# Kernel optimization log

Hardware: AMD Instinct MI355X
Metric: run time of the kernel (lower is better)

## Reference

```python
import jax, jax.numpy as jnp
import numpy as np

VOCAB = 10000
HID = 256

def setup_inputs() -> dict:
    key = jax.random.key(0)
    ks = jax.random.split(key, 7)
    B, T = 64, 64
    input_data = jax.random.randint(ks[0], (B, T), 0, VOCAB, dtype=jnp.int32)
    targets = jax.random.randint(ks[1], (B, T), 0, VOCAB, dtype=jnp.int32)
    # Xavier-ish scaled params
    E = jax.random.normal(ks[2], (VOCAB, HID), dtype=jnp.float32) * (1.0 / np.sqrt(HID))
    W_lstm = jax.random.normal(ks[3], (2 * HID, 4 * HID), dtype=jnp.float32) * (1.0 / np.sqrt(2 * HID))
    b_lstm = jnp.zeros((4 * HID,), dtype=jnp.float32)
    W_dense = jax.random.normal(ks[4], (HID, VOCAB), dtype=jnp.float32) * (1.0 / np.sqrt(HID))
    b_dense = jnp.zeros((VOCAB,), dtype=jnp.float32)
    return {"input_data": input_data, "targets": targets, "E": E,
            "W_lstm": W_lstm, "b_lstm": b_lstm, "W_dense": W_dense, "b_dense": b_dense}

def lstm_scan(xs, W, b, h0, c0):
    # xs: [T, B, H] time-major. TF LSTMCell: gates = [x,h]@W + b, order i,j,f,o, forget_bias=1.0
    def step(carry, x):
        h, c = carry
        gates = jnp.concatenate([x, h], axis=-1) @ W + b  # [B, 4H]
        i, j, f, o = jnp.split(gates, 4, axis=-1)
        c_new = jax.nn.sigmoid(f + 1.0) * c + jax.nn.sigmoid(i) * jnp.tanh(j)
        h_new = jax.nn.sigmoid(o) * jnp.tanh(c_new)
        return (h_new, c_new), h_new
    (hT, cT), hs = jax.lax.scan(step, (h0, c0), xs)
    return hs, (hT, cT)

def reference(input_data, targets, E, W_lstm, b_lstm, W_dense, b_dense):
    B, T = input_data.shape
    inputs = E[input_data]                       # [B, T, H] embedding lookup (no dropout: eval)
    xs = jnp.transpose(inputs, (1, 0, 2))        # [T, B, H]
    h0 = jnp.zeros((B, HID), dtype=E.dtype)
    c0 = jnp.zeros((B, HID), dtype=E.dtype)
    hs, _ = lstm_scan(xs, W_lstm, b_lstm, h0, c0)  # [T, B, H]
    outputs = jnp.transpose(hs, (1, 0, 2))       # [B, T, H]
    logits = outputs @ W_dense + b_dense         # [B, T, V]
    logp = jax.nn.log_softmax(logits, axis=-1)
    ce = -jnp.take_along_axis(logp, targets[..., None].astype(jnp.int32), axis=-1)[..., 0]  # [B, T]
    perplexity = jnp.exp(ce)                     # elementwise, as in add_loss_op
    return perplexity
```

## Files before the change

### kernel.cpp

```cpp
#include <hip/hip_runtime.h>
#include <math.h>

#define VOCABN 10000
#define HIDN   256
#define GATES  1024
#define BN     64
#define TN     64
#define BT     4096
#define NCT    625

typedef unsigned int       u32;
typedef unsigned short     u16;
typedef unsigned long long u64;
typedef float v4f __attribute__((ext_vector_type(4)));
typedef short v8s __attribute__((ext_vector_type(8)));

__device__ __forceinline__ float bf2f(u16 u) {
    return __uint_as_float(((u32)u) << 16);
}
__device__ __forceinline__ u16 f2bf(float f) {
    u32 u = __float_as_uint(f);
    u += 0x7FFFu + ((u >> 16) & 1u);
    return (u16)(u >> 16);
}
__device__ __forceinline__ float fast_sigmoid(float x) {
    return 1.0f / (1.0f + __expf(-x));
}
__device__ __forceinline__ float fast_tanh(float x) {
    float e = __expf(-2.0f * fabsf(x));
    float t = (1.0f - e) / (1.0f + e);
    return copysignf(t, x);
}
__device__ __forceinline__ u64 llc_load(const u64* p) {
    return __hip_atomic_load(p, __ATOMIC_RELAXED, __HIP_MEMORY_SCOPE_AGENT);
}
__device__ __forceinline__ void llc_store(u64* p, u64 v) {
    __hip_atomic_store(p, v, __ATOMIC_RELAXED, __HIP_MEMORY_SCOPE_AGENT);
}
__device__ __forceinline__ u32 cnt_add(u32* p) {
    return __hip_atomic_fetch_add(p, 1u, __ATOMIC_RELAXED,
                                  __HIP_MEMORY_SCOPE_AGENT);
}
__device__ __forceinline__ u32 cnt_read(u32* p) {
    return __hip_atomic_load(p, __ATOMIC_RELAXED, __HIP_MEMORY_SCOPE_AGENT);
}

__device__ __forceinline__ void wfrag_dev(
    const float* __restrict__ src, u16* __restrict__ dst, int ncols, int c,
    int t, u16 lt[HIDN][16])
{
    const float* s = src + (size_t)t * ncols + c * 16;
    #pragma unroll
    for (int j4 = 0; j4 < 4; ++j4) {
        float4 v = *(const float4*)(s + j4 * 4);
        lt[t][j4*4+0] = f2bf(v.x);
        lt[t][j4*4+1] = f2bf(v.y);
        lt[t][j4*4+2] = f2bf(v.z);
        lt[t][j4*4+3] = f2bf(v.w);
    }
    __syncthreads();
    #pragma unroll
    for (int h = 0; h < 2; ++h) {
        int f = t + h * 256;
        int q = f >> 6, l = f & 63;
        int m = l & 15, kb = q * 32 + ((l >> 4) & 3) * 8;
        u32 w[4];
        #pragma unroll
        for (int j = 0; j < 4; ++j)
            w[j] = (u32)lt[kb + 2*j][m] | ((u32)lt[kb + 2*j + 1][m] << 16);
        *(uint4*)(dst + (((size_t)c * 8 + q) * 64 + l) * 8) =
            make_uint4(w[0], w[1], w[2], w[3]);
    }
}

__global__ __launch_bounds__(256) void k_wfrag2(
    const float* __restrict__ W_lstm,
    u16* __restrict__ Wxf, u16* __restrict__ Whf,
    u32* __restrict__ bar)
{
    __shared__ u16 lt[HIDN][16];
    const int bid = blockIdx.x;
    if (bid == 0) bar[threadIdx.x] = 0u;
    if (bid < 64)
        wfrag_dev(W_lstm, Wxf, GATES, bid, threadIdx.x, lt);
    else
        wfrag_dev(W_lstm + (size_t)HIDN * GATES, Whf, GATES, bid - 64,
                  threadIdx.x, lt);
}

__global__ __launch_bounds__(256) void k_wfrag3(
    const float* __restrict__ W_lstm,
    const float* __restrict__ W_dense,
    u16* __restrict__ Wxf, u16* __restrict__ Whf, u16* __restrict__ Wf,
    u32* __restrict__ bar)
{
    __shared__ u16 lt[HIDN][16];
    const int bid = blockIdx.x;
    if (bid == 0) bar[threadIdx.x] = 0u;
    if (bid < 64)
        wfrag_dev(W_lstm, Wxf, GATES, bid, threadIdx.x, lt);
    else if (bid < 128)
        wfrag_dev(W_lstm + (size_t)HIDN * GATES, Whf, GATES, bid - 64,
                  threadIdx.x, lt);
    else
        wfrag_dev(W_dense, Wf, VOCABN, bid - 128, threadIdx.x, lt);
}

__global__ __launch_bounds__(256) void k_wfrag(
    const float* __restrict__ src,
    u16*         __restrict__ dst,
    int ncols)
{
    __shared__ u16 lt[HIDN][16];
    wfrag_dev(src, dst, ncols, blockIdx.x, threadIdx.x, lt);
}

__global__ __launch_bounds__(256) void k_xgates(
    const int*   __restrict__ idx,
    const float* __restrict__ E,
    const u16*   __restrict__ Wxf,
    const float* __restrict__ bl,
    float*       __restrict__ gx)
{
    const int r0   = blockIdx.x * 16;
    const int tid  = threadIdx.x;
    const int w    = tid >> 6, lane = tid & 63;
    const int m    = lane & 15, quad = lane >> 4;

    v8s a[8];
    {
        const float* e = E + (size_t)idx[r0 + m] * HIDN + quad * 8;
        #pragma unroll
        for (int q = 0; q < 8; ++q) {
            float4 x0 = *(const float4*)(e + q * 32);
            float4 x1 = *(const float4*)(e + q * 32 + 4);
            uint4 t4 = make_uint4(
                (u32)f2bf(x0.x) | ((u32)f2bf(x0.y) << 16),
                (u32)f2bf(x0.z) | ((u32)f2bf(x0.w) << 16),
                (u32)f2bf(x1.x) | ((u32)f2bf(x1.y) << 16),
                (u32)f2bf(x1.z) | ((u32)f2bf(x1.w) << 16));
            a[q] = *(v8s*)&t4;
        }
    }

    for (int c = w; c < GATES / 16; c += 4) {
        v4f acc = {0.f, 0.f, 0.f, 0.f};
        #pragma unroll
        for (int q = 0; q < 8; ++q) {
            v8s b = *(const v8s*)(Wxf + (((size_t)c * 8 + q) * 64 + lane) * 8);
            acc = __builtin_amdgcn_mfma_f32_16x16x32_bf16(a[q], b, acc, 0, 0, 0);
        }
        const int col = c * 16 + m;
        const float bv = bl[col];
        #pragma unroll
        for (int r = 0; r < 4; ++r)
            gx[(size_t)(r0 + quad * 4 + r) * GATES + col] = acc[r] + bv;
    }
}

__global__ __launch_bounds__(256) void k_plstm(
    const u16*   __restrict__ Whf,
    const float* __restrict__ gx,
    u16*                      Hx,
    u16*         __restrict__ Hb,
    u32*                      bar)
{
    __shared__ uint4 Wl4[4 * 512];
    __shared__ float gl[4][16][16];

    const int tid  = threadIdx.x;
    const int rg   = blockIdx.x >> 4;
    const int ns   = blockIdx.x & 15;
    const int u0   = ns * 16;
    const int w    = tid >> 6;
    const int lane = tid & 63;
    const int m    = lane & 15, kq = lane >> 4;

    {
        const uint4* src = (const uint4*)Whf;
        #pragma unroll
        for (int i = 0; i < 8; ++i) {
            int e  = tid + i * 256;
            int ct = e >> 9, off = e & 511;
            Wl4[e] = src[(size_t)(ct * 16 + ns) * 512 + off];
        }
    }
    {
        float* g0 = (float*)gl;
        #pragma unroll
        for (int j = 0; j < 4; ++j) g0[tid * 4 + j] = 0.0f;
    }
    __syncthreads();

    const u16* Wl = (const u16*)Wl4;

    const int r = tid >> 4, u = tid & 15;
    const int b = rg * 16 + r;
    const float* gxp = gx + (size_t)b * TN * GATES + u0 + u;
    u16* hbp = Hb + (size_t)b * TN * HIDN + u0 + u;
    const int hxw = b * HIDN + u0 + u;
    const int aoff = (rg * 16 + m) * HIDN + kq * 8;

    float cstate = 0.0f;
    float4 gxr;
    gxr.x = gxp[0]; gxr.y = gxp[256]; gxr.z = gxp[512]; gxr.w = gxp[768];

    for (int t = 0; t < TN; ++t) {
        float4 gxn = gxr;
        if (t + 1 < TN) {
            const float* p = gxp + (size_t)(t + 1) * GATES;
            gxn.x = p[0]; gxn.y = p[256]; gxn.z = p[512]; gxn.w = p[768];
        }

        if (t > 0) {
            const u64* hsrc = (const u64*)(Hx + (t & 1) * (BN * HIDN) + aoff);
            v4f acc = {0.f, 0.f, 0.f, 0.f};
            #pragma unroll
            for (int q = 0; q < 8; ++q) {
                union { u64 d[2]; v8s v; } av;
                av.d[0] = llc_load(hsrc + q * 8);
                av.d[1] = llc_load(hsrc + q * 8 + 1);
                v8s bf = *(const v8s*)(Wl + ((w * 8 + q) * 64 + lane) * 8);
                acc = __builtin_amdgcn_mfma_f32_16x16x32_bf16(av.v, bf, acc, 0, 0, 0);
            }
            #pragma unroll
            for (int rr = 0; rr < 4; ++rr)
                gl[w][kq * 4 + rr][m] = acc[rr];
        }
        __syncthreads();

        {
            float ai = gl[0][r][u] + gxr.x;
            float aj = gl[1][r][u] + gxr.y;
            float af = gl[2][r][u] + gxr.z;
            float ao = gl[3][r][u] + gxr.w;
            float ig = fast_sigmoid(ai);
            float fg = fast_sigmoid(af + 1.0f);
            float og = fast_sigmoid(ao);
            float jt = fast_tanh(aj);
            cstate = fg * cstate + ig * jt;
            float hn = og * fast_tanh(cstate);
            u32 hv = f2bf(hn);
            hbp[(size_t)t * HIDN] = (u16)hv;

            if (t + 1 < TN) {
                u32 p1 = __shfl_down(hv, 1);
                u32 p2 = __shfl_down(hv, 2);
                u32 p3 = __shfl_down(hv, 3);
                if ((tid & 3) == 0) {
                    u64 pk = (u64)(hv | (p1 << 16))
                           | ((u64)(p2 | (p3 << 16)) << 32);
                    u64* dst = (u64*)(Hx + (((t & 1) ^ 1) * (BN * HIDN)) + hxw);
                    llc_store(dst, pk);
                }
            }
        }

        if (t + 1 < TN) {
            __syncthreads();
            if (tid == 0) {
                cnt_add(&bar[rg * 64]);
                u32 tgt = (u32)(t + 1) * 16u;
                while (cnt_read(&bar[rg * 64]) < tgt)
                    __builtin_amdgcn_s_sleep(1);
            }
            __syncthreads();
        }
        gxr = gxn;
    }
}

__global__ __launch_bounds__(256, 1) void k_dense(
    const u16*   __restrict__ Hb,
    const u16*   __restrict__ Wf,
    const float* __restrict__ bd,
    float*       __restrict__ S)
{
    __shared__ float Sl[64];
    const int bid = blockIdx.x;
    const int hv  = bid & 7;
    const int rg  = bid >> 3;
    const int r0  = rg * 64;
    const int tid = threadIdx.x;
    const int w   = tid >> 6, lane = tid & 63;
    const int m   = lane & 15, kq = lane >> 4;

    if (tid < 64) Sl[tid] = 0.0f;

    v8s a[4][8];
    #pragma unroll
    for (int rt = 0; rt < 4; ++rt) {
        const u16* hrow = Hb + (size_t)(r0 + rt * 16 + m) * HIDN + kq * 8;
        #pragma unroll
        for (int q = 0; q < 8; ++q)
            a[rt][q] = *(const v8s*)(hrow + q * 32);
    }
    __syncthreads();

    float s[4][4] = {{0.f,0.f,0.f,0.f},{0.f,0.f,0.f,0.f},
                     {0.f,0.f,0.f,0.f},{0.f,0.f,0.f,0.f}};
    const int cbeg = (hv * NCT) >> 3;
    const int cend = ((hv + 1) * NCT) >> 3;
    for (int c = cbeg + w; c < cend; c += 4) {
        v4f acc[4] = {{0.f,0.f,0.f,0.f},{0.f,0.f,0.f,0.f},
                      {0.f,0.f,0.f,0.f},{0.f,0.f,0.f,0.f}};
        #pragma unroll
        for (int q = 0; q < 8; ++q) {
            v8s bq = *(const v8s*)(Wf + (((size_t)c * 8 + q) * 64 + lane) * 8);
            #pragma unroll
            for (int rt = 0; rt < 4; ++rt)
                acc[rt] = __builtin_amdgcn_mfma_f32_16x16x32_bf16(
                              a[rt][q], bq, acc[rt], 0, 0, 0);
        }
        const float bv = bd[c * 16 + m];
        #pragma unroll
        for (int rt = 0; rt < 4; ++rt)
            #pragma unroll
            for (int r = 0; r < 4; ++r)
                s[rt][r] += __expf(acc[rt][r] + bv);
    }

    #pragma unroll
    for (int rt = 0; rt < 4; ++rt)
        #pragma unroll
        for (int r = 0; r < 4; ++r)
            atomicAdd(&Sl[rt * 16 + kq * 4 + r], s[rt][r]);
    __syncthreads();
    if (tid < 64) S[(size_t)hv * BT + r0 + tid] = Sl[tid];
}

__global__ __launch_bounds__(256) void k_target(
    const u16*   __restrict__ Hb,
    const u16*   __restrict__ Wf,
    const float* __restrict__ bd,
    const int*   __restrict__ tgt,
    const float* __restrict__ S,
    float*       __restrict__ out)
{
    const int tid = threadIdx.x;
    const int row = blockIdx.x * 8 + (tid >> 5);
    const int t   = tid & 31;
    const int q   = t >> 2, lq = t & 3;
    const int v   = tgt[row];
    const int c   = v >> 4, vm = v & 15;
    const int kb  = q * 32 + lq * 8;

    v8s h  = *(const v8s*)(Hb + (size_t)row * HIDN + kb);
    v8s wv = *(const v8s*)(Wf + (((size_t)c * 8 + q) * 64 + lq * 16 + vm) * 8);
    float acc = 0.0f;
    #pragma unroll
    for (int j = 0; j < 8; ++j)
        acc = fmaf(bf2f((u16)h[j]), bf2f((u16)wv[j]), acc);
    #pragma unroll
    for (int off = 16; off >= 1; off >>= 1)
        acc += __shfl_down(acc, off, 32);
    if (t == 0) {
        float tlv = acc + bd[v];
        float sum = 0.0f;
        #pragma unroll
        for (int p = 0; p < 8; ++p) sum += S[(size_t)p * BT + row];
        out[row] = __expf(__logf(sum) - tlv);
    }
}

extern "C" void kernel_launch(void* const* d_in, const int* in_sizes, int n_in,
                              void* d_out, int out_size, void* d_ws, size_t ws_size,
                              hipStream_t stream) {
    const int*   input   = (const int*)  d_in[0];
    const int*   targets = (const int*)  d_in[1];
    const float* E       = (const float*)d_in[2];
    const float* W_lstm  = (const float*)d_in[3];
    const float* b_lstm  = (const float*)d_in[4];
    const float* W_dense = (const float*)d_in[5];
    const float* b_dense = (const float*)d_in[6];
    float* out = (float*)d_out;

    char* ws = (char*)d_ws;
    const bool wide = (ws_size >= ((size_t)25 << 20));

    if (wide) {
        float* gx  = (float*)ws;
        u16*   Wf  = (u16*)(ws + ((size_t)16 << 20));
        u16*   Hb  = (u16*)(ws + ((size_t)21 << 20) + ((size_t)256 << 10));
        u16*   Whf = (u16*)(ws + ((size_t)23 << 20) + ((size_t)256 << 10));
        u16*   Wxf = (u16*)(ws + ((size_t)23 << 20) + ((size_t)768 << 10));
        u16*   Hx  = (u16*)(ws + ((size_t)24 << 20) + ((size_t)256 << 10));
        float* S   = (float*)(ws + ((size_t)24 << 20) + ((size_t)320 << 10));
        u32*   bar = (u32*)  (ws + ((size_t)24 << 20) + ((size_t)448 << 10));

        k_wfrag3<<<753,     256, 0, stream>>>(W_lstm, W_dense, Wxf, Whf, Wf, bar);
        k_xgates<<<BT / 16, 256, 0, stream>>>(input, E, Wxf, b_lstm, gx);
        k_plstm <<<64,      256, 0, stream>>>(Whf, gx, Hx, Hb, bar);
        k_dense <<<512,     256, 0, stream>>>(Hb, Wf, b_dense, S);
        k_target<<<BT / 8,  256, 0, stream>>>(Hb, Wf, b_dense, targets, S, out);
    } else {
        float* gx  = (float*)ws;
        u16*   Wf  = (u16*)ws;
        u16*   Hb  = (u16*)(ws + ((size_t)16 << 20));
        u16*   Whf = (u16*)(ws + ((size_t)18 << 20));
        u16*   Wxf = (u16*)(ws + ((size_t)18 << 20) + ((size_t)512 << 10));
        u16*   Hx  = (u16*)(ws + ((size_t)19 << 20));
        float* S   = (float*)(ws + ((size_t)19 << 20) + ((size_t)64 << 10));
        u32*   bar = (u32*)  (ws + ((size_t)19 << 20) + ((size_t)192 << 10));

        k_wfrag2<<<128,     256, 0, stream>>>(W_lstm, Wxf, Whf, bar);
        k_xgates<<<BT / 16, 256, 0, stream>>>(input, E, Wxf, b_lstm, gx);
        k_plstm <<<64,      256, 0, stream>>>(Whf, gx, Hx, Hb, bar);
        k_wfrag <<<NCT,     256, 0, stream>>>(W_dense, Wf, VOCABN);
        k_dense <<<512,     256, 0, stream>>>(Hb, Wf, b_dense, S);
        k_target<<<BT / 8,  256, 0, stream>>>(Hb, Wf, b_dense, targets, S, out);
    }
}
```

Measured before the change: 360.6 us.

## Replace per-step counter barrier with sentinel-flagged hidden-state ring buffer

The recurrent LSTM kernel no longer uses a global atomic counter barrier with two __syncthreads per timestep. Instead, hidden-state slots in a 4-deep ring buffer are pre-filled with an all-ones sentinel, and consumers spin on the data words themselves until real values arrive. The gate scratch in shared memory is double-buffered so the removed trailing sync does not create a race. This targets the latency of the per-step grid synchronization, at the risk of relying on the sentinel never matching valid bf16 data and on correct ordering of the relaxed atomic stores used to reset slots.

```diff
diff --git a/kernel.cpp b/kernel.cpp
--- a/kernel.cpp
+++ b/kernel.cpp
@@ -15,6 +15,8 @@
 typedef float v4f __attribute__((ext_vector_type(4)));
 typedef short v8s __attribute__((ext_vector_type(8)));
 
+#define SENT 0xFFFFFFFFFFFFFFFFULL
+
 __device__ __forceinline__ float bf2f(u16 u) {
     return __uint_as_float(((u32)u) << 16);
 }
@@ -36,13 +38,6 @@
 }
 __device__ __forceinline__ void llc_store(u64* p, u64 v) {
     __hip_atomic_store(p, v, __ATOMIC_RELAXED, __HIP_MEMORY_SCOPE_AGENT);
-}
-__device__ __forceinline__ u32 cnt_add(u32* p) {
-    return __hip_atomic_fetch_add(p, 1u, __ATOMIC_RELAXED,
-                                  __HIP_MEMORY_SCOPE_AGENT);
-}
-__device__ __forceinline__ u32 cnt_read(u32* p) {
-    return __hip_atomic_load(p, __ATOMIC_RELAXED, __HIP_MEMORY_SCOPE_AGENT);
 }
 
 __device__ __forceinline__ void wfrag_dev(
@@ -76,34 +71,36 @@
 __global__ __launch_bounds__(256) void k_wfrag2(
     const float* __restrict__ W_lstm,
     u16* __restrict__ Wxf, u16* __restrict__ Whf,
-    u32* __restrict__ bar)
+    u64* __restrict__ Hx64)
 {
     __shared__ u16 lt[HIDN][16];
     const int bid = blockIdx.x;
-    if (bid == 0) bar[threadIdx.x] = 0u;
-    if (bid < 64)
+    if (bid < 64) {
+        Hx64[(size_t)bid * 256 + threadIdx.x] = SENT;
         wfrag_dev(W_lstm, Wxf, GATES, bid, threadIdx.x, lt);
-    else
+    } else {
         wfrag_dev(W_lstm + (size_t)HIDN * GATES, Whf, GATES, bid - 64,
                   threadIdx.x, lt);
+    }
 }
 
 __global__ __launch_bounds__(256) void k_wfrag3(
     const float* __restrict__ W_lstm,
     const float* __restrict__ W_dense,
     u16* __restrict__ Wxf, u16* __restrict__ Whf, u16* __restrict__ Wf,
-    u32* __restrict__ bar)
+    u64* __restrict__ Hx64)
 {
     __shared__ u16 lt[HIDN][16];
     const int bid = blockIdx.x;
-    if (bid == 0) bar[threadIdx.x] = 0u;
-    if (bid < 64)
+    if (bid < 64) {
+        Hx64[(size_t)bid * 256 + threadIdx.x] = SENT;
         wfrag_dev(W_lstm, Wxf, GATES, bid, threadIdx.x, lt);
-    else if (bid < 128)
+    } else if (bid < 128) {
         wfrag_dev(W_lstm + (size_t)HIDN * GATES, Whf, GATES, bid - 64,
                   threadIdx.x, lt);
-    else
+    } else {
         wfrag_dev(W_dense, Wf, VOCABN, bid - 128, threadIdx.x, lt);
+    }
 }
 
 __global__ __launch_bounds__(256) void k_wfrag(
@@ -162,11 +159,10 @@
     const u16*   __restrict__ Whf,
     const float* __restrict__ gx,
     u16*                      Hx,
-    u16*         __restrict__ Hb,
-    u32*                      bar)
+    u16*         __restrict__ Hb)
 {
     __shared__ uint4 Wl4[4 * 512];
-    __shared__ float gl[4][16][16];
+    __shared__ float gl[2][4][16][16];
 
     const int tid  = threadIdx.x;
     const int rg   = blockIdx.x >> 4;
@@ -186,7 +182,7 @@
         }
     }
     {
-        float* g0 = (float*)gl;
+        float* g0 = (float*)gl[0];
         #pragma unroll
         for (int j = 0; j < 4; ++j) g0[tid * 4 + j] = 0.0f;
     }
@@ -200,6 +196,8 @@
     u16* hbp = Hb + (size_t)b * TN * HIDN + u0 + u;
     const int hxw = b * HIDN + u0 + u;
     const int aoff = (rg * 16 + m) * HIDN + kq * 8;
+    u64* const hx64 = (u64*)Hx;
+    const int cidx = (rg * 16 + (tid >> 2)) * (HIDN / 4) + ns * 4 + (tid & 3);
 
     float cstate = 0.0f;
     float4 gxr;
@@ -212,28 +210,45 @@
             gxn.x = p[0]; gxn.y = p[256]; gxn.z = p[512]; gxn.w = p[768];
         }
 
+        if (t + 1 < TN && tid < 64)
+            llc_store(hx64 + (size_t)((t + 1) & 3) * (BN * HIDN / 4) + cidx,
+                      SENT);
+
         if (t > 0) {
-            const u64* hsrc = (const u64*)(Hx + (t & 1) * (BN * HIDN) + aoff);
+            const u64* hsrc =
+                (const u64*)(Hx + (size_t)((t - 1) & 3) * (BN * HIDN) + aoff);
+            u64 d[16];
+            #pragma unroll
+            for (int q = 0; q < 8; ++q) {
+                d[2 * q]     = llc_load(hsrc + q * 8);
+                d[2 * q + 1] = llc_load(hsrc + q * 8 + 1);
+            }
+            #pragma unroll
+            for (int i = 0; i < 16; ++i)
+                while (d[i] == SENT)
+                    d[i] = llc_load(hsrc + (i >> 1) * 8 + (i & 1));
+
             v4f acc = {0.f, 0.f, 0.f, 0.f};
             #pragma unroll
             for (int q = 0; q < 8; ++q) {
-                union { u64 d[2]; v8s v; } av;
-                av.d[0] = llc_load(hsrc + q * 8);
-                av.d[1] = llc_load(hsrc + q * 8 + 1);
+                union { u64 dd[2]; v8s v; } av;
+                av.dd[0] = d[2 * q];
+                av.dd[1] = d[2 * q + 1];
                 v8s bf = *(const v8s*)(Wl + ((w * 8 + q) * 64 + lane) * 8);
-                acc = __builtin_amdgcn_mfma_f32_16x16x32_bf16(av.v, bf, acc, 0, 0, 0);
+                acc = __builtin_amdgcn_mfma_f32_16x16x32_bf16(av.v, bf, acc,
+                                                              0, 0, 0);
             }
             #pragma unroll
             for (int rr = 0; rr < 4; ++rr)
-                gl[w][kq * 4 + rr][m] = acc[rr];
+                gl[t & 1][w][kq * 4 + rr][m] = acc[rr];
         }
         __syncthreads();
 
         {
-            float ai = gl[0][r][u] + gxr.x;
-            float aj = gl[1][r][u] + gxr.y;
-            float af = gl[2][r][u] + gxr.z;
-            float ao = gl[3][r][u] + gxr.w;
+            float ai = gl[t & 1][0][r][u] + gxr.x;
+            float aj = gl[t & 1][1][r][u] + gxr.y;
+            float af = gl[t & 1][2][r][u] + gxr.z;
+            float ao = gl[t & 1][3][r][u] + gxr.w;
             float ig = fast_sigmoid(ai);
             float fg = fast_sigmoid(af + 1.0f);
             float og = fast_sigmoid(ao);
@@ -250,21 +265,11 @@
                 if ((tid & 3) == 0) {
                     u64 pk = (u64)(hv | (p1 << 16))
                            | ((u64)(p2 | (p3 << 16)) << 32);
-                    u64* dst = (u64*)(Hx + (((t & 1) ^ 1) * (BN * HIDN)) + hxw);
+                    u64* dst =
+                        (u64*)(Hx + (size_t)(t & 3) * (BN * HIDN) + hxw);
                     llc_store(dst, pk);
                 }
             }
-        }
-
-        if (t + 1 < TN) {
-            __syncthreads();
-            if (tid == 0) {
-                cnt_add(&bar[rg * 64]);
-                u32 tgt = (u32)(t + 1) * 16u;
-                while (cnt_read(&bar[rg * 64]) < tgt)
-                    __builtin_amdgcn_s_sleep(1);
-            }
-            __syncthreads();
         }
         gxr = gxn;
     }
@@ -385,12 +390,12 @@
         u16*   Whf = (u16*)(ws + ((size_t)23 << 20) + ((size_t)256 << 10));
         u16*   Wxf = (u16*)(ws + ((size_t)23 << 20) + ((size_t)768 << 10));
         u16*   Hx  = (u16*)(ws + ((size_t)24 << 20) + ((size_t)256 << 10));
-        float* S   = (float*)(ws + ((size_t)24 << 20) + ((size_t)320 << 10));
-        u32*   bar = (u32*)  (ws + ((size_t)24 << 20) + ((size_t)448 << 10));
-
-        k_wfrag3<<<753,     256, 0, stream>>>(W_lstm, W_dense, Wxf, Whf, Wf, bar);
+        float* S   = (float*)(ws + ((size_t)24 << 20) + ((size_t)384 << 10));
+
+        k_wfrag3<<<753,     256, 0, stream>>>(W_lstm, W_dense, Wxf, Whf, Wf,
+                                              (u64*)Hx);
         k_xgates<<<BT / 16, 256, 0, stream>>>(input, E, Wxf, b_lstm, gx);
-        k_plstm <<<64,      256, 0, stream>>>(Whf, gx, Hx, Hb, bar);
+        k_plstm <<<64,      256, 0, stream>>>(Whf, gx, Hx, Hb);
         k_dense <<<512,     256, 0, stream>>>(Hb, Wf, b_dense, S);
         k_target<<<BT / 8,  256, 0, stream>>>(Hb, Wf, b_dense, targets, S, out);
     } else {
@@ -400,12 +405,11 @@
         u16*   Whf = (u16*)(ws + ((size_t)18 << 20));
         u16*   Wxf = (u16*)(ws + ((size_t)18 << 20) + ((size_t)512 << 10));
         u16*   Hx  = (u16*)(ws + ((size_t)19 << 20));
-        float* S   = (float*)(ws + ((size_t)19 << 20) + ((size_t)64 << 10));
-        u32*   bar = (u32*)  (ws + ((size_t)19 << 20) + ((size_t)192 << 10));
-
-        k_wfrag2<<<128,     256, 0, stream>>>(W_lstm, Wxf, Whf, bar);
+        float* S   = (float*)(ws + ((size_t)19 << 20) + ((size_t)128 << 10));
+
+        k_wfrag2<<<128,     256, 0, stream>>>(W_lstm, Wxf, Whf, (u64*)Hx);
         k_xgates<<<BT / 16, 256, 0, stream>>>(input, E, Wxf, b_lstm, gx);
-        k_plstm <<<64,      256, 0, stream>>>(Whf, gx, Hx, Hb, bar);
+        k_plstm <<<64,      256, 0, stream>>>(Whf, gx, Hx, Hb);
         k_wfrag <<<NCT,     256, 0, stream>>>(W_dense, Wf, VOCABN);
         k_dense <<<512,     256, 0, stream>>>(Hb, Wf, b_dense, S);
         k_target<<<BT / 8,  256, 0, stream>>>(Hb, Wf, b_dense, targets, S, out);
```

Result: slower. 407.9 us (+13.1%).
